# Kernel tuning notes

Measured on AMD Instinct MI355X. Metric: run time of the kernel, lower is better.

Reference implementation:

```python
import math
import jax, jax.numpy as jnp
import numpy as np

BLOCK = 32          # hard-coded in the CUDA kernels
NUM_HEADS = 16
NUM_BLOCKS = 512    # (max_pos//32) * block_per_row = 128 * 4
DIAG_N = 3
FIRST_N = 0


def _mra2_attention(Q, K, V, mask):
    # Q,K,V: (meta_batch, seq, head_dim); mask: (meta_batch, seq) in {0,1}
    mb, seq_len, d = Q.shape
    bs = BLOCK
    nb = seq_len // bs
    scale = 1.0 / math.sqrt(d)
    Q = Q * mask[:, :, None]
    K = K * mask[:, :, None]
    V = V * mask[:, :, None]

    # ---- low resolution block means (mask-weighted), approx_mode='full' keeps V_hat
    tc = mask.reshape(mb, nb, bs).sum(-1)                 # token count per block
    denom = tc[:, :, None] + 1e-6
    Q_hat = Q.reshape(mb, nb, bs, d).sum(2) / denom       # (mb, nb, d)
    K_hat = K.reshape(mb, nb, bs, d).sum(2) / denom
    V_hat = V.reshape(mb, nb, bs, d).sum(2) / denom
    low_logit = jnp.einsum('bid,bjd->bij', Q_hat, K_hat) * scale
    row_max = low_logit.max(-1, keepdims=True)            # before mask subtraction
    low_logit = low_logit - 10000.0 * ((tc[:, None, :] * tc[:, :, None]) < 0.5).astype(Q.dtype)

    # ---- block index selection (torch runs this under no_grad)
    lrn = jax.lax.stop_gradient(low_logit - row_max)
    if DIAG_N > 0:
        off = DIAG_N // 2
        i = jnp.arange(nb)
        band = (jnp.abs(i[:, None] - i[None, :]) <= off).astype(Q.dtype)
        lrn = lrn + band[None] * 5000.0
    if FIRST_N > 0:
        lrn = lrn.at[:, :FIRST_N, :].add(5000.0)
        lrn = lrn.at[:, :, :FIRST_N].add(5000.0)
    top_vals, indices = jax.lax.top_k(lrn.reshape(mb, nb * nb), NUM_BLOCKS)
    threshold = top_vals.min(-1)
    high_mask = (lrn >= threshold[:, None, None]).astype(Q.dtype)  # selected-block mask

    q_blk = indices // nb                                  # (mb, n) query block ids
    k_blk = indices % nb                                   # (mb, n) key block ids
    Qs = jnp.take_along_axis(Q.reshape(mb, nb, bs, d), q_blk[:, :, None, None], axis=1)
    Ks = jnp.take_along_axis(K.reshape(mb, nb, bs, d), k_blk[:, :, None, None], axis=1)
    Vs = jnp.take_along_axis(V.reshape(mb, nb, bs, d), k_blk[:, :, None, None], axis=1)

    # sampled dense-dense: sparse_C[b,n,k,q] (key-in-block, query-in-block layout as in kernel)
    hi_logit = jnp.einsum('bnkd,bnqd->bnkq', Ks, Qs) * scale

    # per query-row max over selected blocks (kernel index_max; constant for grad)
    b_idx = jnp.arange(mb)[:, None]
    blk_max = hi_logit.max(axis=2)                         # (mb, n, bs) max over key axis
    max_blocks = jnp.full((mb, nb, bs), -1e8, Q.dtype).at[b_idx, q_blk].max(blk_max)
    max_blocks = jax.lax.stop_gradient(max_blocks)
    max_vals = max_blocks.reshape(mb, seq_len)
    max_scatter = jnp.take_along_axis(max_blocks, q_blk[:, :, None], axis=1)[:, :, None, :]

    # key-side mask per selected block (sparse_mask_B)
    mask_blk = jnp.take_along_axis(mask.reshape(mb, nb, bs), k_blk[:, :, None], axis=1)
    hi_attn = jnp.exp(hi_logit - max_scatter - 10000.0 * (1.0 - mask_blk[:, :, :, None]))

    # sparse-dense matmul + reduce-sum normalizer, scattered back per query block
    hi_out = jnp.zeros((mb, nb, bs, d), Q.dtype).at[b_idx, q_blk].add(
        jnp.einsum('bnkq,bnkd->bnqd', hi_attn, Vs)).reshape(mb, seq_len, d)
    hi_norm = jnp.zeros((mb, nb, bs), Q.dtype).at[b_idx, q_blk].add(
        hi_attn.sum(axis=2)).reshape(mb, seq_len)

    # ---- low resolution branch, selected blocks suppressed via high_mask
    low_attn = jnp.exp(low_logit - row_max - 10000.0 * high_mask) * tc[:, None, :]
    low_out = jnp.repeat(jnp.einsum('bij,bjd->bid', low_attn, V_hat), bs, axis=1)
    low_norm = jnp.repeat(low_attn.sum(-1), bs, axis=1)

    log_corr = (jnp.repeat(row_max[:, :, 0], bs, axis=1) - max_vals) * mask
    low_corr = jnp.exp(jnp.minimum(log_corr, 0.0))
    hi_corr = jnp.exp(-jnp.maximum(log_corr, 0.0))

    ctx = hi_out * hi_corr[:, :, None] + low_out * low_corr[:, :, None]
    ctx = ctx / (hi_norm * hi_corr + low_norm * low_corr + 1e-6)[:, :, None]
    return ctx * mask[:, :, None]


def _forward(hidden_states, attention_mask, w_q, b_q, w_k, b_k, w_v, b_v):
    b, s, hdim = hidden_states.shape
    h = NUM_HEADS
    dh = hdim // h

    def split_heads(x):
        return x.reshape(b, s, h, dh).transpose(0, 2, 1, 3).reshape(b * h, s, dh)

    q = split_heads(hidden_states @ w_q.T + b_q)
    k = split_heads(hidden_states @ w_k.T + b_k)
    v = split_heads(hidden_states @ w_v.T + b_v)
    # invert extended additive mask (1 + am/10000) and replicate over heads
    # (torch's .repeat(1, h, 1).reshape(b*h, s) stacks h copies of the [b,s] mask)
    mask = jnp.tile(1.0 + attention_mask / 10000.0, (h, 1))
    ctx = _mra2_attention(q, k, v, mask)
    ctx = ctx.reshape(b, h, s, dh).transpose(0, 2, 1, 3).reshape(b, s, hdim)
    return ctx


def setup_inputs() -> dict:
    key = jax.random.key(0)
    ks = jax.random.split(key, 4)
    H = 1024
    return {
        'hidden_states': jax.random.normal(ks[0], (2, 4096, H), jnp.float32),
        'attention_mask': jnp.zeros((2, 4096), jnp.float32),
        'w_q': jax.random.normal(ks[1], (H, H), jnp.float32) * 0.02,
        'b_q': jnp.zeros((H,), jnp.float32),
        'w_k': jax.random.normal(ks[2], (H, H), jnp.float32) * 0.02,
        'b_k': jnp.zeros((H,), jnp.float32),
        'w_v': jax.random.normal(ks[3], (H, H), jnp.float32) * 0.02,
        'b_v': jnp.zeros((H,), jnp.float32),
    }


def reference(hidden_states, attention_mask, w_q, b_q, w_k, b_k, w_v, b_v):
    return _forward(hidden_states, attention_mask, w_q, b_q, w_k, b_k, w_v, b_v)
```

## Files before the change

kernel.cpp:

```cpp
#include <hip/hip_runtime.h>
#include <cstdint>
#include <cstddef>

#define MAXSEL 160
static constexpr int S    = 4096;
static constexpr int H    = 1024;
static constexpr int DH   = 64;
static constexpr int NB   = 128;
static constexpr int MBH  = 32;
static constexpr int M8   = 8192;
static constexpr int N3   = 3072;

typedef _Float16 half8 __attribute__((ext_vector_type(8)));
typedef _Float16 half4v __attribute__((ext_vector_type(4)));
typedef float floatx4 __attribute__((ext_vector_type(4)));

__device__ __forceinline__ void load_lds16(const void* g, void* l) {
  __builtin_amdgcn_global_load_lds((const __attribute__((address_space(1))) unsigned int*)g,
                                   (__attribute__((address_space(3))) unsigned int*)l,
                                   16, 0, 0);
}

__global__ __launch_bounds__(256) void k_prep(const float* __restrict__ hidden,
                                              const float* __restrict__ am,
                                              const float* __restrict__ wq,
                                              const float* __restrict__ wk,
                                              const float* __restrict__ wv,
                                              _Float16* __restrict__ h16,
                                              _Float16* __restrict__ w16,
                                              _Float16* __restrict__ wlo,
                                              _Float16* __restrict__ hb_hi,
                                              _Float16* __restrict__ hb_lo,
                                              float* __restrict__ tcv,
                                              int* __restrict__ selcnt) {
  const int blk_id = blockIdx.x;
  if (blk_id < 256) {
    if (blk_id == 0) {
      for (int i = threadIdx.x; i < MBH * NB; i += 256) selcnt[i] = 0;
    }
    int b2 = blk_id >> 7, blk = blk_id & 127;
    int c = threadIdx.x * 4;
    float4 s0 = make_float4(0.f, 0.f, 0.f, 0.f);
    float4 s1 = make_float4(0.f, 0.f, 0.f, 0.f);
    for (int i = 0; i < 32; i += 4) {
      int pos0 = blk * 32 + i;
      size_t base = ((size_t)b2 * 4096 + pos0) * 1024 + c;
      const float4 x0 = *(const float4*)&hidden[base];
      const float4 x1 = *(const float4*)&hidden[base + 1024];
      const float4 x2 = *(const float4*)&hidden[base + 2048];
      const float4 x3 = *(const float4*)&hidden[base + 3072];
      float a00 = am[pos0],      a01 = am[pos0 + 1],      a02 = am[pos0 + 2],      a03 = am[pos0 + 3];
      float a10 = am[4096+pos0], a11 = am[4096+pos0 + 1], a12 = am[4096+pos0 + 2], a13 = am[4096+pos0 + 3];
      half4v h;
      h[0]=(_Float16)x0.x; h[1]=(_Float16)x0.y; h[2]=(_Float16)x0.z; h[3]=(_Float16)x0.w;
      *(half4v*)&h16[base] = h;
      h[0]=(_Float16)x1.x; h[1]=(_Float16)x1.y; h[2]=(_Float16)x1.z; h[3]=(_Float16)x1.w;
      *(half4v*)&h16[base + 1024] = h;
      h[0]=(_Float16)x2.x; h[1]=(_Float16)x2.y; h[2]=(_Float16)x2.z; h[3]=(_Float16)x2.w;
      *(half4v*)&h16[base + 2048] = h;
      h[0]=(_Float16)x3.x; h[1]=(_Float16)x3.y; h[2]=(_Float16)x3.z; h[3]=(_Float16)x3.w;
      *(half4v*)&h16[base + 3072] = h;
      float m0, m1;
      m0 = 1.f + a00 * 1e-4f; m1 = 1.f + a10 * 1e-4f;
      s0.x += m0*x0.x; s0.y += m0*x0.y; s0.z += m0*x0.z; s0.w += m0*x0.w;
      s1.x += m1*x0.x; s1.y += m1*x0.y; s1.z += m1*x0.z; s1.w += m1*x0.w;
      m0 = 1.f + a01 * 1e-4f; m1 = 1.f + a11 * 1e-4f;
      s0.x += m0*x1.x; s0.y += m0*x1.y; s0.z += m0*x1.z; s0.w += m0*x1.w;
      s1.x += m1*x1.x; s1.y += m1*x1.y; s1.z += m1*x1.z; s1.w += m1*x1.w;
      m0 = 1.f + a02 * 1e-4f; m1 = 1.f + a12 * 1e-4f;
      s0.x += m0*x2.x; s0.y += m0*x2.y; s0.z += m0*x2.z; s0.w += m0*x2.w;
      s1.x += m1*x2.x; s1.y += m1*x2.y; s1.z += m1*x2.z; s1.w += m1*x2.w;
      m0 = 1.f + a03 * 1e-4f; m1 = 1.f + a13 * 1e-4f;
      s0.x += m0*x3.x; s0.y += m0*x3.y; s0.z += m0*x3.z; s0.w += m0*x3.w;
      s1.x += m1*x3.x; s1.y += m1*x3.y; s1.z += m1*x3.z; s1.w += m1*x3.w;
    }
    size_t row0 = (size_t)(b2 * 2 + 0) * 128 + blk;
    size_t row1 = (size_t)(b2 * 2 + 1) * 128 + blk;
    half4v hi, lo;
    hi[0]=(_Float16)s0.x; lo[0]=(_Float16)(s0.x-(float)hi[0]);
    hi[1]=(_Float16)s0.y; lo[1]=(_Float16)(s0.y-(float)hi[1]);
    hi[2]=(_Float16)s0.z; lo[2]=(_Float16)(s0.z-(float)hi[2]);
    hi[3]=(_Float16)s0.w; lo[3]=(_Float16)(s0.w-(float)hi[3]);
    *(half4v*)&hb_hi[row0 * 1024 + c] = hi;
    *(half4v*)&hb_lo[row0 * 1024 + c] = lo;
    hi[0]=(_Float16)s1.x; lo[0]=(_Float16)(s1.x-(float)hi[0]);
    hi[1]=(_Float16)s1.y; lo[1]=(_Float16)(s1.y-(float)hi[1]);
    hi[2]=(_Float16)s1.z; lo[2]=(_Float16)(s1.z-(float)hi[2]);
    hi[3]=(_Float16)s1.w; lo[3]=(_Float16)(s1.w-(float)hi[3]);
    *(half4v*)&hb_hi[row1 * 1024 + c] = hi;
    *(half4v*)&hb_lo[row1 * 1024 + c] = lo;
    if (b2 == 0 && threadIdx.x == 0) {
      float t0 = 0.f, t1 = 0.f;
      for (int i = 0; i < 32; ++i) {
        int pos = blk * 32 + i;
        t0 += 1.f + am[pos] * 1e-4f;
        t1 += 1.f + am[4096 + pos] * 1e-4f;
      }
      tcv[blk] = t0; tcv[128 + blk] = t1;
    }
  } else {
    long j = (long)(blk_id - 256) * 256 + threadIdx.x;
    const long NW4 = (long)H * H / 4;
    int which = (int)(j / NW4);
    long jj = j - (long)which * NW4;
    const float* src = which == 0 ? wq : (which == 1 ? wk : wv);
    float4 x = ((const float4*)src)[jj];
    half4v h;
    h[0] = (_Float16)x.x; h[1] = (_Float16)x.y;
    h[2] = (_Float16)x.z; h[3] = (_Float16)x.w;
    *(half4v*)&w16[j * 4] = h;
    if (which < 2) {
      half4v r;
      r[0] = (_Float16)(x.x - (float)h[0]);
      r[1] = (_Float16)(x.y - (float)h[1]);
      r[2] = (_Float16)(x.z - (float)h[2]);
      r[3] = (_Float16)(x.w - (float)h[3]);
      *(half4v*)&wlo[j * 4] = r;
    }
  }
}

__global__ __launch_bounds__(512, 4) void k_gemm_qkv(const _Float16* __restrict__ A,
                                                     const _Float16* __restrict__ B,
                                                     const float* __restrict__ bq,
                                                     const float* __restrict__ bk,
                                                     const float* __restrict__ bv,
                                                     const float* __restrict__ am,
                                                     _Float16* __restrict__ q16,
                                                     _Float16* __restrict__ k16,
                                                     _Float16* __restrict__ v16,
                                                     const _Float16* __restrict__ Ahi,
                                                     const _Float16* __restrict__ Alo,
                                                     const _Float16* __restrict__ Blo,
                                                     float* __restrict__ sideQK) {
  __shared__ _Float16 sh[36864];

  if (blockIdx.x < 768) {
    const int id = blockIdx.x;
    const int swz = (id & 7) * 96 + (id >> 3);
    const int by = swz / 12;
    const int bx = swz - by * 12;
    const int tid = threadIdx.x;
    const int lane = tid & 63, wv = tid >> 6;
    const int wm = wv >> 2, wn = wv & 3;
    const int l15 = lane & 15, quad = lane >> 4;

    _Float16* As = sh;
    _Float16* Bs = sh + 12288;

    floatx4 acc[4][4] = {};

    const _Float16* Ag = A + (size_t)(by * 128) * 1024;
    const _Float16* Bg = B + (size_t)(bx * 256) * 1024;

    const int gr  = lane >> 2;
    const int gcb = ((lane & 3) ^ ((lane >> 3) & 3)) * 8;
    const _Float16* agl  = Ag + (size_t)(wv * 16 + gr) * 1024 + gcb;
    const _Float16* bgl0 = Bg + (size_t)(wv * 32 + gr) * 1024 + gcb;
    const _Float16* bgl1 = Bg + (size_t)(wv * 32 + 16 + gr) * 1024 + gcb;
    const int aw  = (wv * 16) * 32;
    const int bw0 = (wv * 32) * 32;
    const int bw1 = (wv * 32 + 16) * 32;

#define STAGE(TT, BB)                                                   \
    {                                                                   \
      load_lds16(agl  + (size_t)(TT) * 32, &As[(BB) * 4096 + aw]);      \
      load_lds16(bgl0 + (size_t)(TT) * 32, &Bs[(BB) * 8192 + bw0]);     \
      load_lds16(bgl1 + (size_t)(TT) * 32, &Bs[(BB) * 8192 + bw1]);     \
    }

    STAGE(0, 0)
    STAGE(1, 1)

    const int rc = ((quad ^ ((l15 >> 1) & 3)) << 3);

#pragma unroll
    for (int t = 0; t < 32; ++t) {
      if (t == 31) { asm volatile("s_waitcnt vmcnt(0)" ::: "memory"); }
      else         { asm volatile("s_waitcnt vmcnt(3)" ::: "memory"); }
      __builtin_amdgcn_s_barrier();
      if (t < 30) {
        const int nb = (t + 2) % 3;
        STAGE(t + 2, nb)
      }
      const int bb = t % 3;
      half8 a[4], b[4];
#pragma unroll
      for (int mt = 0; mt < 4; ++mt)
        a[mt] = *(const half8*)&As[bb * 4096 + (wm * 64 + mt * 16 + l15) * 32 + rc];
#pragma unroll
      for (int nt = 0; nt < 4; ++nt)
        b[nt] = *(const half8*)&Bs[bb * 8192 + (wn * 64 + nt * 16 + l15) * 32 + rc];
      __builtin_amdgcn_s_setprio(1);
#pragma unroll
      for (int mt = 0; mt < 4; ++mt)
#pragma unroll
        for (int nt = 0; nt < 4; ++nt)
          acc[mt][nt] = __builtin_amdgcn_mfma_f32_16x16x32_f16(a[mt], b[nt], acc[mt][nt], 0, 0, 0);
      __builtin_amdgcn_s_setprio(0);
    }
#undef STAGE

    const int which = bx >> 2;
    const float* bias = which == 0 ? bq : (which == 1 ? bk : bv);
    _Float16* dst = which == 0 ? q16 : (which == 1 ? k16 : v16);
    const int hh = (bx & 3) * 4 + wn;
    const int m2 = hh & 1;
#pragma unroll
    for (int nt = 0; nt < 4; ++nt) {
      const int dd = nt * 16 + l15;
      const float bsv = bias[hh * 64 + dd];
#pragma unroll
      for (int mt = 0; mt < 4; ++mt) {
#pragma unroll
        for (int r = 0; r < 4; ++r) {
          int srow = by * 128 + wm * 64 + mt * 16 + quad * 4 + r;
          int b2 = srow >> 12, s = srow & 4095;
          float mv = 1.f + am[m2 * 4096 + s] * 1e-4f;
          float v = (acc[mt][nt][r] + bsv) * mv;
          int mb = b2 * 16 + hh;
          dst[((size_t)mb * 4096 + s) * 64 + dd] = (_Float16)v;
        }
      }
    }
    return;
  }

  const int half = threadIdx.x >> 8;
  const int stid = threadIdx.x & 255;
  const int sb   = (blockIdx.x - 768) * 2 + half;
  const int slane = stid & 63, swv = stid >> 6;
  const int kk  = sb >> 8;
  const int sbb = sb & 255;
  const int sbx = sbb & 31;
  const int sby = sbb >> 5;
  const int swm = swv >> 1, swn = swv & 1;
  const int sl15 = slane & 15, squad = slane >> 4;
  _Float16* base = sh + half * 16384;
  _Float16* sAhi = base;
  _Float16* sAlo = base + 4096;
  _Float16* sBhi = base + 8192;
  _Float16* sBlo = base + 12288;

  floatx4 acc[2][2] = {};

  const int srow = slane >> 3;
  const int scol = (((slane & 7) ^ (srow & 7)) * 8);
  const int sswz = sl15 & 7;
  const _Float16* src;
  _Float16* dst;
  if      (swv == 0) { src = Ahi + (size_t)(sby * 64) * 1024; dst = sAhi; }
  else if (swv == 1) { src = Alo + (size_t)(sby * 64) * 1024; dst = sAlo; }
  else if (swv == 2) { src = B   + (size_t)(sbx * 64) * 1024; dst = sBhi; }
  else               { src = Blo + (size_t)(sbx * 64) * 1024; dst = sBlo; }

  const int kbeg = kk * 512;
  for (int k0 = kbeg; k0 < kbeg + 512; k0 += 64) {
    __syncthreads();
#pragma unroll
    for (int i = 0; i < 8; ++i)
      load_lds16(src + (size_t)(i * 8 + srow) * 1024 + k0 + scol, dst + i * 512);
    __syncthreads();
#pragma unroll
    for (int ks = 0; ks < 2; ++ks) {
      const int kc = ks * 4;
      half8 ah[2], al[2], bh[2], bl[2];
#pragma unroll
      for (int mt = 0; mt < 2; ++mt) {
        int off = (swm * 32 + mt * 16 + sl15) * 64 + (((kc + squad) ^ sswz) << 3);
        ah[mt] = *(const half8*)&sAhi[off];
        al[mt] = *(const half8*)&sAlo[off];
      }
#pragma unroll
      for (int nt = 0; nt < 2; ++nt) {
        int off = (swn * 32 + nt * 16 + sl15) * 64 + (((kc + squad) ^ sswz) << 3);
        bh[nt] = *(const half8*)&sBhi[off];
        bl[nt] = *(const half8*)&sBlo[off];
      }
#pragma unroll
      for (int mt = 0; mt < 2; ++mt)
#pragma unroll
        for (int nt = 0; nt < 2; ++nt) {
          acc[mt][nt] = __builtin_amdgcn_mfma_f32_16x16x32_f16(ah[mt], bh[nt], acc[mt][nt], 0, 0, 0);
          acc[mt][nt] = __builtin_amdgcn_mfma_f32_16x16x32_f16(ah[mt], bl[nt], acc[mt][nt], 0, 0, 0);
          acc[mt][nt] = __builtin_amdgcn_mfma_f32_16x16x32_f16(al[mt], bh[nt], acc[mt][nt], 0, 0, 0);
        }
    }
  }
  float* outp = sideQK + (size_t)kk * (512 * 2048);
#pragma unroll
  for (int mt = 0; mt < 2; ++mt)
#pragma unroll
    for (int nt = 0; nt < 2; ++nt)
#pragma unroll
      for (int rr = 0; rr < 4; ++rr) {
        int row = sby * 64 + swm * 32 + mt * 16 + squad * 4 + rr;
        int col = sbx * 64 + swn * 32 + nt * 16 + sl15;
        outp[(size_t)row * 2048 + col] = acc[mt][nt][rr];
      }
}

__global__ __launch_bounds__(256) void k_lowlogit(const float* __restrict__ sideQK,
                                                  const float* __restrict__ tcv,
                                                  const float* __restrict__ bq,
                                                  const float* __restrict__ bk,
                                                  float* __restrict__ ll,
                                                  float* __restrict__ rmaxout,
                                                  const _Float16* __restrict__ v16,
                                                  float* __restrict__ vhat,
                                                  _Float16* __restrict__ v16T) {
  __shared__ __attribute__((aligned(16))) char shraw[37376];
  const int tid = threadIdx.x;

  if (blockIdx.x >= 256) {
    const int lane = tid & 63, wv = tid >> 6;
    _Float16* Vs = (_Float16*)shraw + wv * 2304;
    int bid = (blockIdx.x - 256) * 4 + wv;
    int mb = bid >> 7, blk = bid & 127;
    const _Float16* src = v16 + ((size_t)mb * 4096 + blk * 32) * 64;
    int r = lane >> 3, c = (lane & 7) * 8;
#pragma unroll
    for (int it = 0; it < 4; ++it)
      *(uint4*)&Vs[(it * 8 + r) * 72 + c] = *(const uint4*)&src[(it * 8 + r) * 64 + c];
    __syncthreads();
    float acc = 0.f;
    half8 col[4];
#pragma unroll
    for (int k = 0; k < 32; ++k) {
      _Float16 x = Vs[k * 72 + lane];
      col[k >> 3][k & 7] = x;
      acc += (float)x;
    }
    vhat[(size_t)bid * 64 + lane] = acc / (tcv[(mb & 1) * 128 + blk] + 1e-6f);
    _Float16* dst = v16T + (size_t)(mb * 64 + lane) * 4096 + blk * 32;
#pragma unroll
    for (int p = 0; p < 4; ++p) *(half8*)&dst[p * 8] = col[p];
    return;
  }

  const int mb = blockIdx.x >> 3;
  const int ib = blockIdx.x & 7;
  const int b2 = mb >> 4, m2 = mb & 1, hh = mb & 15;
  const int combo = b2 * 2 + m2;
  float* Kh  = (float*)shraw;
  float* Qh  = (float*)(shraw + 32768);
  float* tcL = (float*)(shraw + 32768 + 4096);

  const float* P1 = sideQK + (size_t)512 * 2048;

  if (tid < 128) tcL[tid] = tcv[m2 * 128 + tid];
  __syncthreads();
#pragma unroll
  for (int i = 0; i < 8; ++i) {
    int ci = tid + i * 256;
    int row = ci >> 4, c4 = (ci & 15) * 4;
    float tck = tcL[row];
    float den = 1.f / (tck + 1e-6f);
    size_t idx = ((size_t)combo * 128 + row) * 2048 + 1024 + hh * 64 + c4;
    float4 x0 = *(const float4*)&sideQK[idx];
    float4 x1 = *(const float4*)&P1[idx];
    float4 bb = *(const float4*)&bk[hh * 64 + c4];
    float4 o;
    o.x = (x0.x + x1.x + bb.x * tck) * den; o.y = (x0.y + x1.y + bb.y * tck) * den;
    o.z = (x0.z + x1.z + bb.z * tck) * den; o.w = (x0.w + x1.w + bb.w * tck) * den;
    *(float4*)&Kh[row * 64 + c4] = o;
  }
  {
    int row = tid >> 4, c4 = (tid & 15) * 4;
    int gi = ib * 16 + row;
    float tcq = tcL[gi];
    float den = 1.f / (tcq + 1e-6f);
    size_t idx = ((size_t)combo * 128 + gi) * 2048 + hh * 64 + c4;
    float4 x0 = *(const float4*)&sideQK[idx];
    float4 x1 = *(const float4*)&P1[idx];
    float4 bb = *(const float4*)&bq[hh * 64 + c4];
    float4 o;
    o.x = (x0.x + x1.x + bb.x * tcq) * den; o.y = (x0.y + x1.y + bb.y * tcq) * den;
    o.z = (x0.z + x1.z + bb.z * tcq) * den; o.w = (x0.w + x1.w + bb.w * tcq) * den;
    *(float4*)&Qh[row * 64 + c4] = o;
  }
  __syncthreads();

  const int il = tid >> 4, jg = tid & 15;
  const int i = ib * 16 + il;
  float tcq = tcL[i];
  float dots[8] = {};
#pragma unroll
  for (int dd = 0; dd < 16; ++dd) {
    int d4 = ((dd + tid) & 15) * 4;
    float4 qv = *(const float4*)&Qh[il * 64 + d4];
#pragma unroll
    for (int jj = 0; jj < 8; ++jj) {
      float4 kv = *(const float4*)&Kh[(jg * 8 + jj) * 64 + d4];
      dots[jj] += qv.x * kv.x + qv.y * kv.y + qv.z * kv.z + qv.w * kv.w;
    }
  }
  float tmax = -1e30f;
#pragma unroll
  for (int jj = 0; jj < 8; ++jj) {
    int j = jg * 8 + jj;
    float raw = dots[jj] * 0.125f;
    tmax = fmaxf(tmax, raw);
    float pen = (tcq * tcL[j] < 0.5f) ? 10000.f : 0.f;
    ll[(size_t)mb * 16384 + (size_t)i * 128 + j] = raw - pen;
  }
#pragma unroll
  for (int mk = 1; mk < 16; mk <<= 1) tmax = fmaxf(tmax, __shfl_xor(tmax, mk));
  if (jg == 0) rmaxout[mb * 128 + i] = tmax;
}

__global__ __launch_bounds__(256) void k_topk(const float* __restrict__ ll,
                                              const float* __restrict__ rmax,
                                              float* __restrict__ thr,
                                              int* __restrict__ selcnt,
                                              int* __restrict__ selkb) {
  const int mb = blockIdx.x;
  const int t = threadIdx.x;
  const int wid = t >> 6;
  __shared__ int red2[2][4];

  unsigned code[64];
#pragma unroll
  for (int j = 0; j < 64; ++j) {
    int e = j * 256 + t;
    int i = e >> 7, jj = e & 127;
    float lrn = ll[(size_t)mb * 16384 + e] - rmax[mb * 128 + i];
    int di = i - jj;
    if (di <= 1 && di >= -1) lrn += 5000.f;
    unsigned b = __float_as_uint(lrn);
    code[j] = (b & 0x80000000u) ? ~b : (b | 0x80000000u);
  }

  unsigned lo = 0u, hi = 0xFFFFFFFFu;
  for (int it = 0; it < 32; ++it) {
    unsigned mid = lo + ((hi - lo) >> 1);
    int c = 0;
#pragma unroll
    for (int j = 0; j < 64; ++j) c += (code[j] >= mid) ? 1 : 0;
#pragma unroll
    for (int mk = 1; mk < 64; mk <<= 1) c += __shfl_xor(c, mk);
    if ((t & 63) == 0) red2[it & 1][wid] = c;
    __syncthreads();
    int total = red2[it & 1][0] + red2[it & 1][1] + red2[it & 1][2] + red2[it & 1][3];
    if (total >= 512) lo = mid; else hi = mid;
  }
  if (t == 0) {
    unsigned bits = (lo & 0x80000000u) ? (lo & 0x7FFFFFFFu) : ~lo;
    thr[mb] = __uint_as_float(bits);
  }
#pragma unroll
  for (int j = 0; j < 64; ++j) {
    if (code[j] >= lo) {
      int e = j * 256 + t;
      int i = e >> 7, jj = e & 127;
      int slot = atomicAdd(&selcnt[mb * 128 + i], 1);
      if (slot < MAXSEL) selkb[(size_t)(mb * 128 + i) * MAXSEL + slot] = jj;
    }
  }
}

__global__ __launch_bounds__(64) void k_hi(const _Float16* __restrict__ q16,
                                           const _Float16* __restrict__ k16,
                                           const _Float16* __restrict__ v16T,
                                           const int* __restrict__ selcnt,
                                           const int* __restrict__ selkb,
                                           const float* __restrict__ rmax,
                                           const float* __restrict__ thr,
                                           const float* __restrict__ tcv,
                                           const float* __restrict__ vhat,
                                           const float* __restrict__ ll,
                                           const float* __restrict__ am,
                                           float* __restrict__ out) {
  const int mb = blockIdx.x & 31, qb = blockIdx.x >> 5;
  const int sid = mb * 128 + qb;
  const int lane = threadIdx.x;
  const int l15 = lane & 15, quad = lane >> 4;
  const int m2 = mb & 1, b2 = mb >> 4, hh = mb & 15;

  __shared__ _Float16 Ps[32 * 40];

  const _Float16* qbase = q16 + ((size_t)mb * 4096 + qb * 32) * 64;
  half8 aq[2][2];
#pragma unroll
  for (int mt = 0; mt < 2; ++mt)
#pragma unroll
    for (int ks = 0; ks < 2; ++ks)
      aq[mt][ks] = *(const half8*)&qbase[(mt * 16 + l15) * 64 + ks * 32 + quad * 8];

  const float rmaxb = rmax[sid];
  const float th = thr[mb];
  float accL = 0.f, nrmL = 0.f;
#pragma unroll 4
  for (int j = 0; j < 128; ++j) {
    float llv = ll[(size_t)mb * 16384 + (size_t)qb * 128 + j];
    float lrn = llv - rmaxb;
    int di = qb - j;
    if (di <= 1 && di >= -1) lrn += 5000.f;
    float w = (lrn >= th) ? 0.f : __expf(llv - rmaxb) * tcv[m2 * 128 + j];
    accL += w * vhat[((size_t)(mb * 128 + j)) * 64 + lane];
    nrmL += w;
  }

  int nk = selcnt[sid];
  if (nk > MAXSEL) nk = MAXSEL;
  const int* list = selkb + (size_t)sid * MAXSEL;

  const _Float16* kbase  = k16  + (size_t)mb * 4096 * 64;
  const _Float16* vtbase = v16T + (size_t)mb * 64 * 4096;

  float rm[2][4];
  floatx4 o[2][4] = {};
  floatx4 onrm[2] = {};
#pragma unroll
  for (int mt = 0; mt < 2; ++mt)
#pragma unroll
    for (int r = 0; r < 4; ++r) rm[mt][r] = -1e8f;

  half8 ones;
#pragma unroll
  for (int j = 0; j < 8; ++j) ones[j] = (_Float16)1.f;

  for (int t = 0; t < nk; ++t) {
    const int kb = list[t];
    const _Float16* kp = kbase + (size_t)kb * 32 * 64;
    half8 b0[2], b1[2];
#pragma unroll
    for (int ks = 0; ks < 2; ++ks) {
      b0[ks] = *(const half8*)&kp[(l15) * 64 + ks * 32 + quad * 8];
      b1[ks] = *(const half8*)&kp[(16 + l15) * 64 + ks * 32 + quad * 8];
    }
    const _Float16* vp = vtbase + kb * 32 + quad * 8;
    half8 vb0 = *(const half8*)&vp[(size_t)(l15) * 4096];
    half8 vb1 = *(const half8*)&vp[(size_t)(16 + l15) * 4096];
    half8 vb2 = *(const half8*)&vp[(size_t)(32 + l15) * 4096];
    half8 vb3 = *(const half8*)&vp[(size_t)(48 + l15) * 4096];

    floatx4 sf[2][2] = {};
    sf[0][0] = __builtin_amdgcn_mfma_f32_16x16x32_f16(aq[0][0], b0[0], sf[0][0], 0, 0, 0);
    sf[0][0] = __builtin_amdgcn_mfma_f32_16x16x32_f16(aq[0][1], b0[1], sf[0][0], 0, 0, 0);
    sf[0][1] = __builtin_amdgcn_mfma_f32_16x16x32_f16(aq[0][0], b1[0], sf[0][1], 0, 0, 0);
    sf[0][1] = __builtin_amdgcn_mfma_f32_16x16x32_f16(aq[0][1], b1[1], sf[0][1], 0, 0, 0);
    sf[1][0] = __builtin_amdgcn_mfma_f32_16x16x32_f16(aq[1][0], b0[0], sf[1][0], 0, 0, 0);
    sf[1][0] = __builtin_amdgcn_mfma_f32_16x16x32_f16(aq[1][1], b0[1], sf[1][0], 0, 0, 0);
    sf[1][1] = __builtin_amdgcn_mfma_f32_16x16x32_f16(aq[1][0], b1[0], sf[1][1], 0, 0, 0);
    sf[1][1] = __builtin_amdgcn_mfma_f32_16x16x32_f16(aq[1][1], b1[1], sf[1][1], 0, 0, 0);

    float pen0, pen1;
    {
      float mk0 = 1.f + am[m2 * 4096 + kb * 32 + l15] * 1e-4f;
      float mk1 = 1.f + am[m2 * 4096 + kb * 32 + 16 + l15] * 1e-4f;
      pen0 = 10000.f * (1.f - mk0);
      pen1 = 10000.f * (1.f - mk1);
    }
#pragma unroll
    for (int mt = 0; mt < 2; ++mt)
#pragma unroll
      for (int r = 0; r < 4; ++r) {
        float s0 = sf[mt][0][r] * 0.125f;
        float s1 = sf[mt][1][r] * 0.125f;
        float v = fmaxf(s0, s1);
#pragma unroll
        for (int mk = 1; mk < 16; mk <<= 1) v = fmaxf(v, __shfl_xor(v, mk));
        float mnew  = fmaxf(rm[mt][r], v);
        float alpha = __expf(rm[mt][r] - mnew);
        rm[mt][r] = mnew;
        float p0 = __expf(s0 - mnew - pen0);
        float p1 = __expf(s1 - mnew - pen1);
        o[mt][0][r] *= alpha; o[mt][1][r] *= alpha;
        o[mt][2][r] *= alpha; o[mt][3][r] *= alpha;
        onrm[mt][r] *= alpha;
        int row = mt * 16 + quad * 4 + r;
        Ps[row * 40 + l15] = (_Float16)p0;
        Ps[row * 40 + 16 + l15] = (_Float16)p1;
      }
    __syncthreads();
    half8 pa0 = *(const half8*)&Ps[(l15) * 40 + quad * 8];
    half8 pa1 = *(const half8*)&Ps[(16 + l15) * 40 + quad * 8];
    o[0][0] = __builtin_amdgcn_mfma_f32_16x16x32_f16(pa0, vb0, o[0][0], 0, 0, 0);
    o[0][1] = __builtin_amdgcn_mfma_f32_16x16x32_f16(pa0, vb1, o[0][1], 0, 0, 0);
    o[0][2] = __builtin_amdgcn_mfma_f32_16x16x32_f16(pa0, vb2, o[0][2], 0, 0, 0);
    o[0][3] = __builtin_amdgcn_mfma_f32_16x16x32_f16(pa0, vb3, o[0][3], 0, 0, 0);
    o[1][0] = __builtin_amdgcn_mfma_f32_16x16x32_f16(pa1, vb0, o[1][0], 0, 0, 0);
    o[1][1] = __builtin_amdgcn_mfma_f32_16x16x32_f16(pa1, vb1, o[1][1], 0, 0, 0);
    o[1][2] = __builtin_amdgcn_mfma_f32_16x16x32_f16(pa1, vb2, o[1][2], 0, 0, 0);
    o[1][3] = __builtin_amdgcn_mfma_f32_16x16x32_f16(pa1, vb3, o[1][3], 0, 0, 0);
    onrm[0] = __builtin_amdgcn_mfma_f32_16x16x32_f16(pa0, ones, onrm[0], 0, 0, 0);
    onrm[1] = __builtin_amdgcn_mfma_f32_16x16x32_f16(pa1, ones, onrm[1], 0, 0, 0);
    __syncthreads();
  }

  float lo_d[4];
#pragma unroll
  for (int ntd = 0; ntd < 4; ++ntd) lo_d[ntd] = __shfl(accL, ntd * 16 + l15);
#pragma unroll
  for (int mt = 0; mt < 2; ++mt) {
#pragma unroll
    for (int r = 0; r < 4; ++r) {
      int q = mt * 16 + quad * 4 + r;
      int qpos = qb * 32 + q;
      float mq = 1.f + am[m2 * 4096 + qpos] * 1e-4f;
      float logc = (rmaxb - rm[mt][r]) * mq;
      float lc = __expf(fminf(logc, 0.f));
      float hc = __expf(-fmaxf(logc, 0.f));
      float den = onrm[mt][r] * hc + nrmL * lc + 1e-6f;
      float sc = mq / den;
#pragma unroll
      for (int ntd = 0; ntd < 4; ++ntd) {
        float val = (o[mt][ntd][r] * hc + lo_d[ntd] * lc) * sc;
        out[((size_t)b2 * 4096 + qpos) * 1024 + hh * 64 + ntd * 16 + l15] = val;
      }
    }
  }
}

extern "C" void kernel_launch(void* const* d_in, const int* in_sizes, int n_in,
                              void* d_out, int out_size, void* d_ws, size_t ws_size,
                              hipStream_t stream) {
  const float* hidden = (const float*)d_in[0];
  const float* am     = (const float*)d_in[1];
  const float* wq     = (const float*)d_in[2];
  const float* bq     = (const float*)d_in[3];
  const float* wk     = (const float*)d_in[4];
  const float* bk     = (const float*)d_in[5];
  const float* wv     = (const float*)d_in[6];
  const float* bv     = (const float*)d_in[7];
  float* out = (float*)d_out;

  char* ws = (char*)d_ws;
  size_t off = 0;
  auto alloc = [&](size_t bytes) -> char* {
    char* p = ws + off;
    off += (bytes + 255) & ~(size_t)255;
    return p;
  };
  _Float16* h16    = (_Float16*)alloc((size_t)M8 * H * 2);
  _Float16* w16    = (_Float16*)alloc((size_t)N3 * H * 2);
  _Float16* wlo    = (_Float16*)alloc((size_t)2 * H * H * 2);
  _Float16* q16    = (_Float16*)alloc((size_t)MBH * S * DH * 2);
  _Float16* k16    = (_Float16*)alloc((size_t)MBH * S * DH * 2);
  _Float16* v16    = (_Float16*)alloc((size_t)MBH * S * DH * 2);
  _Float16* hb_hi  = (_Float16*)alloc((size_t)4 * NB * H * 2);
  _Float16* hb_lo  = (_Float16*)alloc((size_t)4 * NB * H * 2);
  float* tcv       = (float*)alloc((size_t)2 * NB * 4);
  float* sideQK    = (float*)alloc((size_t)2 * 512 * 2048 * 4);
  float* ll        = (float*)alloc((size_t)MBH * NB * NB * 4);
  float* rmax      = (float*)alloc((size_t)MBH * NB * 4);
  float* thr       = (float*)alloc((size_t)MBH * 4);
  int*   selcnt    = (int*)alloc((size_t)MBH * NB * 4);
  int*   selkb     = (int*)alloc((size_t)MBH * NB * MAXSEL * 4);
  float* vhat      = (float*)alloc((size_t)MBH * NB * DH * 4);
  _Float16* v16T   = h16;

  k_prep<<<dim3(3328), dim3(256), 0, stream>>>(hidden, am, wq, wk, wv,
                                               h16, w16, wlo, hb_hi, hb_lo, tcv, selcnt);
  k_gemm_qkv<<<dim3(1024), dim3(512), 0, stream>>>(h16, w16, bq, bk, bv, am,
                                                   q16, k16, v16,
                                                   hb_hi, hb_lo, wlo, sideQK);
  k_lowlogit<<<dim3(1280), dim3(256), 0, stream>>>(sideQK, tcv, bq, bk, ll, rmax,
                                                   v16, vhat, v16T);
  k_topk<<<dim3(32), dim3(256), 0, stream>>>(ll, rmax, thr, selcnt, selkb);
  k_hi<<<dim3(4096), dim3(64), 0, stream>>>(q16, k16, v16T, selcnt, selkb, rmax, thr,
                                            tcv, vhat, ll, am, out);
}
```

Before: 295.2 us.

## Split k_hi key blocks across four waves and store V transposed per block

Each query block in k_hi is now handled by four waves instead of one. The waves stride over the selected key blocks and the low-resolution loop, and their flash-attention state is merged through shared memory with max-rescaling. The per-iteration __syncthreads becomes a wave-local LDS wait, since each wave has its own P tile. V-transpose storage changes to a contiguous 64x32 tile per key block, so the V loads are compact instead of strided by 4096. The cost is a shared-memory merge step and more shared memory per block.

```diff
diff --git a/kernel.cpp b/kernel.cpp
--- a/kernel.cpp
+++ b/kernel.cpp
@@ -332,7 +332,7 @@
       acc += (float)x;
     }
     vhat[(size_t)bid * 64 + lane] = acc / (tcv[(mb & 1) * 128 + blk] + 1e-6f);
-    _Float16* dst = v16T + (size_t)(mb * 64 + lane) * 4096 + blk * 32;
+    _Float16* dst = v16T + ((size_t)(mb * 128 + blk) * 64 + lane) * 32;
 #pragma unroll
     for (int p = 0; p < 4; ++p) *(half8*)&dst[p * 8] = col[p];
     return;
@@ -459,25 +459,27 @@
   }
 }
 
-__global__ __launch_bounds__(64) void k_hi(const _Float16* __restrict__ q16,
-                                           const _Float16* __restrict__ k16,
-                                           const _Float16* __restrict__ v16T,
-                                           const int* __restrict__ selcnt,
-                                           const int* __restrict__ selkb,
-                                           const float* __restrict__ rmax,
-                                           const float* __restrict__ thr,
-                                           const float* __restrict__ tcv,
-                                           const float* __restrict__ vhat,
-                                           const float* __restrict__ ll,
-                                           const float* __restrict__ am,
-                                           float* __restrict__ out) {
+__global__ __launch_bounds__(256) void k_hi(const _Float16* __restrict__ q16,
+                                            const _Float16* __restrict__ k16,
+                                            const _Float16* __restrict__ v16T,
+                                            const int* __restrict__ selcnt,
+                                            const int* __restrict__ selkb,
+                                            const float* __restrict__ rmax,
+                                            const float* __restrict__ thr,
+                                            const float* __restrict__ tcv,
+                                            const float* __restrict__ vhat,
+                                            const float* __restrict__ ll,
+                                            const float* __restrict__ am,
+                                            float* __restrict__ out) {
   const int mb = blockIdx.x & 31, qb = blockIdx.x >> 5;
   const int sid = mb * 128 + qb;
-  const int lane = threadIdx.x;
+  const int tid = threadIdx.x;
+  const int lane = tid & 63, wid = tid >> 6;
   const int l15 = lane & 15, quad = lane >> 4;
   const int m2 = mb & 1, b2 = mb >> 4, hh = mb & 15;
 
-  __shared__ _Float16 Ps[32 * 40];
+  __shared__ _Float16 Ps[4][32 * 40];
+  __shared__ float mrg[3][64][50];
 
   const _Float16* qbase = q16 + ((size_t)mb * 4096 + qb * 32) * 64;
   half8 aq[2][2];
@@ -491,7 +493,7 @@
   const float th = thr[mb];
   float accL = 0.f, nrmL = 0.f;
 #pragma unroll 4
-  for (int j = 0; j < 128; ++j) {
+  for (int j = wid * 32; j < wid * 32 + 32; ++j) {
     float llv = ll[(size_t)mb * 16384 + (size_t)qb * 128 + j];
     float lrn = llv - rmaxb;
     int di = qb - j;
@@ -506,7 +508,7 @@
   const int* list = selkb + (size_t)sid * MAXSEL;
 
   const _Float16* kbase  = k16  + (size_t)mb * 4096 * 64;
-  const _Float16* vtbase = v16T + (size_t)mb * 64 * 4096;
+  const _Float16* vtbase = v16T + (size_t)mb * 128 * 2048;
 
   float rm[2][4];
   floatx4 o[2][4] = {};
@@ -520,7 +522,9 @@
 #pragma unroll
   for (int j = 0; j < 8; ++j) ones[j] = (_Float16)1.f;
 
-  for (int t = 0; t < nk; ++t) {
+  _Float16* myPs = &Ps[wid][0];
+
+  for (int t = wid; t < nk; t += 4) {
     const int kb = list[t];
     const _Float16* kp = kbase + (size_t)kb * 32 * 64;
     half8 b0[2], b1[2];
@@ -529,11 +533,11 @@
       b0[ks] = *(const half8*)&kp[(l15) * 64 + ks * 32 + quad * 8];
       b1[ks] = *(const half8*)&kp[(16 + l15) * 64 + ks * 32 + quad * 8];
     }
-    const _Float16* vp = vtbase + kb * 32 + quad * 8;
-    half8 vb0 = *(const half8*)&vp[(size_t)(l15) * 4096];
-    half8 vb1 = *(const half8*)&vp[(size_t)(16 + l15) * 4096];
-    half8 vb2 = *(const half8*)&vp[(size_t)(32 + l15) * 4096];
-    half8 vb3 = *(const half8*)&vp[(size_t)(48 + l15) * 4096];
+    const _Float16* vp = vtbase + kb * 2048 + quad * 8;
+    half8 vb0 = *(const half8*)&vp[(l15) * 32];
+    half8 vb1 = *(const half8*)&vp[(16 + l15) * 32];
+    half8 vb2 = *(const half8*)&vp[(32 + l15) * 32];
+    half8 vb3 = *(const half8*)&vp[(48 + l15) * 32];
 
     floatx4 sf[2][2] = {};
     sf[0][0] = __builtin_amdgcn_mfma_f32_16x16x32_f16(aq[0][0], b0[0], sf[0][0], 0, 0, 0);
@@ -570,12 +574,14 @@
         o[mt][2][r] *= alpha; o[mt][3][r] *= alpha;
         onrm[mt][r] *= alpha;
         int row = mt * 16 + quad * 4 + r;
-        Ps[row * 40 + l15] = (_Float16)p0;
-        Ps[row * 40 + 16 + l15] = (_Float16)p1;
-      }
-    __syncthreads();
-    half8 pa0 = *(const half8*)&Ps[(l15) * 40 + quad * 8];
-    half8 pa1 = *(const half8*)&Ps[(16 + l15) * 40 + quad * 8];
+        myPs[row * 40 + l15] = (_Float16)p0;
+        myPs[row * 40 + 16 + l15] = (_Float16)p1;
+      }
+    __builtin_amdgcn_sched_barrier(0);
+    asm volatile("s_waitcnt lgkmcnt(0)" ::: "memory");
+    __builtin_amdgcn_sched_barrier(0);
+    half8 pa0 = *(const half8*)&myPs[(l15) * 40 + quad * 8];
+    half8 pa1 = *(const half8*)&myPs[(16 + l15) * 40 + quad * 8];
     o[0][0] = __builtin_amdgcn_mfma_f32_16x16x32_f16(pa0, vb0, o[0][0], 0, 0, 0);
     o[0][1] = __builtin_amdgcn_mfma_f32_16x16x32_f16(pa0, vb1, o[0][1], 0, 0, 0);
     o[0][2] = __builtin_amdgcn_mfma_f32_16x16x32_f16(pa0, vb2, o[0][2], 0, 0, 0);
@@ -586,7 +592,44 @@
     o[1][3] = __builtin_amdgcn_mfma_f32_16x16x32_f16(pa1, vb3, o[1][3], 0, 0, 0);
     onrm[0] = __builtin_amdgcn_mfma_f32_16x16x32_f16(pa0, ones, onrm[0], 0, 0, 0);
     onrm[1] = __builtin_amdgcn_mfma_f32_16x16x32_f16(pa1, ones, onrm[1], 0, 0, 0);
-    __syncthreads();
+  }
+
+  if (wid > 0) {
+    float* st = &mrg[wid - 1][lane][0];
+#pragma unroll
+    for (int mt = 0; mt < 2; ++mt)
+#pragma unroll
+      for (int r = 0; r < 4; ++r) {
+#pragma unroll
+        for (int ntd = 0; ntd < 4; ++ntd) st[mt * 16 + ntd * 4 + r] = o[mt][ntd][r];
+        st[32 + mt * 4 + r] = onrm[mt][r];
+        st[40 + mt * 4 + r] = rm[mt][r];
+      }
+    st[48] = accL;
+    st[49] = nrmL;
+  }
+  __syncthreads();
+  if (wid != 0) return;
+
+#pragma unroll
+  for (int w = 0; w < 3; ++w) {
+    const float* st = &mrg[w][lane][0];
+    accL += st[48];
+    nrmL += st[49];
+#pragma unroll
+    for (int mt = 0; mt < 2; ++mt)
+#pragma unroll
+      for (int r = 0; r < 4; ++r) {
+        float rmw = st[40 + mt * 4 + r];
+        float mnew = fmaxf(rm[mt][r], rmw);
+        float a0 = __expf(rm[mt][r] - mnew);
+        float a1 = __expf(rmw - mnew);
+        rm[mt][r] = mnew;
+#pragma unroll
+        for (int ntd = 0; ntd < 4; ++ntd)
+          o[mt][ntd][r] = o[mt][ntd][r] * a0 + st[mt * 16 + ntd * 4 + r] * a1;
+        onrm[mt][r] = onrm[mt][r] * a0 + st[32 + mt * 4 + r] * a1;
+      }
   }
 
   float lo_d[4];
@@ -659,6 +702,6 @@
   k_lowlogit<<<dim3(1280), dim3(256), 0, stream>>>(sideQK, tcv, bq, bk, ll, rmax,
                                                    v16, vhat, v16T);
   k_topk<<<dim3(32), dim3(256), 0, stream>>>(ll, rmax, thr, selcnt, selkb);
-  k_hi<<<dim3(4096), dim3(64), 0, stream>>>(q16, k16, v16T, selcnt, selkb, rmax, thr,
-                                            tcv, vhat, ll, am, out);
+  k_hi<<<dim3(4096), dim3(256), 0, stream>>>(q16, k16, v16T, selcnt, selkb, rmax, thr,
+                                             tcv, vhat, ll, am, out);
 }
```

After: 341.0 us. 15.5% more time.
